# Kernel optimization log

Measured on AMD Instinct MI355X. Metric: run time of the kernel, lower is better.

The kernel has to match this reference:

```python
import jax, jax.numpy as jnp
import numpy as np

N, E = 50000, 400000
FN, FE = 128, 128          # in/out node and edge feature dims
W = 256                     # fnns_width
EPS = 1e-5


def _layer_norm(x, g, b):
    m = x.mean(-1, keepdims=True)
    var = x.var(-1, keepdims=True)
    return (x - m) / jnp.sqrt(var + EPS) * g + b


def _fnn(x, params):
    # FNN applies ReLU after EVERY linear, including the last one.
    for w, b in params:
        x = jax.nn.relu(x @ w + b)
    return x


def setup_inputs() -> dict:
    key = jax.random.key(0)
    ks = jax.random.split(key, 32)
    s = 0.05
    d = {
        'v': jax.random.normal(ks[0], (N, FN), jnp.float32),
        'e': jax.random.normal(ks[1], (E, FE), jnp.float32),
        'edge_index': jax.random.randint(ks[2], (2, E), 0, N, jnp.int32),
        # edge branch: LayerNorm over concat width FE + 2*FN = 384
        'edge_ln_g': jnp.ones((FE + 2 * FN,), jnp.float32),
        'edge_ln_b': jnp.zeros((FE + 2 * FN,), jnp.float32),
        'ew0': jax.random.normal(ks[3], (FE + 2 * FN, W), jnp.float32) * s,
        'eb0': jnp.zeros((W,), jnp.float32),
        'ew1': jax.random.normal(ks[4], (W, W), jnp.float32) * s,
        'eb1': jnp.zeros((W,), jnp.float32),
        'ew2': jax.random.normal(ks[5], (W, FE), jnp.float32) * s,
        'eb2': jnp.zeros((FE,), jnp.float32),
        'edge_linear': jax.random.normal(ks[6], (FE, FE), jnp.float32) * s,
        # node branch: LayerNorm over concat width FE + FN = 256
        'node_ln_g': jnp.ones((FE + FN,), jnp.float32),
        'node_ln_b': jnp.zeros((FE + FN,), jnp.float32),
        'nw0': jax.random.normal(ks[7], (FE + FN, W), jnp.float32) * s,
        'nb0': jnp.zeros((W,), jnp.float32),
        'nw1': jax.random.normal(ks[8], (W, W), jnp.float32) * s,
        'nb1': jnp.zeros((W,), jnp.float32),
        'nw2': jax.random.normal(ks[9], (W, FN), jnp.float32) * s,
        'nb2': jnp.zeros((FN,), jnp.float32),
        'node_linear': jax.random.normal(ks[10], (FN, FN), jnp.float32) * s,
    }
    return d


def reference(v, e, edge_index, edge_ln_g, edge_ln_b, ew0, eb0, ew1, eb1,
              ew2, eb2, edge_linear, node_ln_g, node_ln_b, nw0, nb0, nw1,
              nb1, nw2, nb2, node_linear):
    row, col = edge_index[0], edge_index[1]
    n = v.shape[0]
    # edge update: residual linear + FNN(LayerNorm(concat))
    edge_in = jnp.concatenate([e, v[row], v[col]], axis=-1)  # [E, 384]
    e_new = e @ edge_linear + _fnn(
        _layer_norm(edge_in, edge_ln_g, edge_ln_b),
        [(ew0, eb0), (ew1, eb1), (ew2, eb2)])
    # mean scatter-aggregate over destination nodes (col)
    counts = jax.ops.segment_sum(jnp.ones((e.shape[0],), e.dtype), col,
                                 num_segments=n)
    e_aggr = jax.ops.segment_sum(e_new, col, num_segments=n)
    e_aggr = e_aggr / jnp.clip(counts, 1.0)[:, None]
    # node update
    node_in = jnp.concatenate([e_aggr, v], axis=-1)  # [N, 256]
    v_new = v @ node_linear + _fnn(
        _layer_norm(node_in, node_ln_g, node_ln_b),
        [(nw0, nb0), (nw1, nb1), (nw2, nb2)])
    return (v_new, e_new)
```

## Files before the change

kernel.cpp:

```cpp
#include <hip/hip_runtime.h>

typedef _Float16 f16_t;
typedef f16_t f16x4 __attribute__((ext_vector_type(4)));
typedef f16_t f16x8 __attribute__((ext_vector_type(8)));
typedef float f32x4 __attribute__((ext_vector_type(4)));

#define MFMA16(a, b, c) __builtin_amdgcn_mfma_f32_16x16x32_f16((a), (b), (c), 0, 0, 0)

__device__ __forceinline__ float bfr(float x) { return (float)(__bf16)x; }

__global__ void pack_weights_kernel(
    const float* __restrict__ ew0, const float* __restrict__ ew1,
    const float* __restrict__ ew2, const float* __restrict__ eL,
    const float* __restrict__ nw0, const float* __restrict__ nw1,
    const float* __restrict__ nw2, const float* __restrict__ nL,
    f16_t* __restrict__ dst)
{
    int tid = blockIdx.x * 256 + threadIdx.x;
    int fid = tid >> 6, lane = tid & 63;
    const float* src; int Ncols, foff, doff;
    if (fid < 192)      { src = ew0; Ncols = 256; foff = 0;   doff = 0;      }
    else if (fid < 320) { src = ew1; Ncols = 256; foff = 192; doff = 98304;  }
    else if (fid < 384) { src = ew2; Ncols = 128; foff = 320; doff = 163840; }
    else if (fid < 416) { src = eL;  Ncols = 128; foff = 384; doff = 196608; }
    else if (fid < 544) { src = nw0; Ncols = 256; foff = 416; doff = 212992; }
    else if (fid < 672) { src = nw1; Ncols = 256; foff = 544; doff = 278528; }
    else if (fid < 736) { src = nw2; Ncols = 128; foff = 672; doff = 344064; }
    else                { src = nL;  Ncols = 128; foff = 736; doff = 376832; }
    int f = fid - foff;
    int NT = Ncols >> 4;
    int kstep = f / NT, ntile = f - kstep * NT;
    int col = ntile * 16 + (lane & 15);
    int kbase = kstep * 32 + ((lane >> 4) << 3);
    f16x8 out;
    #pragma unroll
    for (int j = 0; j < 8; ++j)
        out[j] = (f16_t)bfr(src[(size_t)(kbase + j) * Ncols + col]);
    *reinterpret_cast<f16x8*>(dst + (size_t)doff + ((size_t)f * 64 + lane) * 8) = out;
}

__global__ void pack_params_kernel(
    const float* __restrict__ elng, const float* __restrict__ elnb,
    const float* __restrict__ eb0,  const float* __restrict__ eb1,
    const float* __restrict__ eb2,  const float* __restrict__ nlng,
    const float* __restrict__ nlnb, const float* __restrict__ nb0,
    const float* __restrict__ nb1,  const float* __restrict__ nb2,
    float* __restrict__ pp)
{
    int tid = blockIdx.x * 256 + threadIdx.x;
    if (tid >= 2560) return;
    const float* src; int off;
    if (tid < 384)       { src = elng; off = 0; }
    else if (tid < 768)  { src = elnb; off = 384; }
    else if (tid < 1024) { src = eb0;  off = 768; }
    else if (tid < 1280) { src = eb1;  off = 1024; }
    else if (tid < 1408) { src = eb2;  off = 1280; }
    else if (tid < 1664) { src = nlng; off = 1408; }
    else if (tid < 1920) { src = nlnb; off = 1664; }
    else if (tid < 2176) { src = nb0;  off = 1920; }
    else if (tid < 2432) { src = nb1;  off = 2176; }
    else                 { src = nb2;  off = 2432; }
    pp[tid] = bfr(src[tid - off]);
}

__launch_bounds__(1024, 8)
__global__ void edge_kernel(
    const float* __restrict__ vfeat, const float* __restrict__ efeat,
    const int* __restrict__ eidx,
    const float* __restrict__ pp,
    const f16_t* __restrict__ pw,
    float* __restrict__ out_e, float* __restrict__ aggr, float* __restrict__ cnts,
    int Ee)
{
    __shared__ f16_t XF[12 * 4 * 512];
    __shared__ f16_t ERF[4 * 4 * 512];
    __shared__ float SB[64 * 8];
    __shared__ int cidx[64];

    const int t    = threadIdx.x;
    const int lane = t & 63;
    const int wv   = t >> 6;
    const int r16  = lane & 15;
    const int g4i  = lane >> 4;
    const size_t ebase = (size_t)blockIdx.x * 64;

    const int et_  = wv >> 2;
    const int sq4  = wv & 3;
    const int edge = et_ * 16 + r16;
    const int slot = sq4 * 4 + g4i;
    const size_t eg0 = ebase + edge;
    const int r0 = eidx[eg0];
    const int c0 = eidx[(size_t)Ee + eg0];

    f16x8 oct[3];
    float s = 0.f, sq = 0.f;
    {
        const float4* e4 = (const float4*)efeat;
        const float4* v4 = (const float4*)vfeat;
        const float4* srcs[3];
        srcs[0] = &e4[eg0 * 32 + slot * 2];
        srcs[1] = &v4[(size_t)r0 * 32 + slot * 2];
        srcs[2] = &v4[(size_t)c0 * 32 + slot * 2];
        #pragma unroll
        for (int i = 0; i < 3; ++i) {
            float4 f0 = srcs[i][0];
            float4 f1 = srcs[i][1];
            float x0 = bfr(f0.x), x1 = bfr(f0.y), x2 = bfr(f0.z), x3 = bfr(f0.w);
            float x4 = bfr(f1.x), x5 = bfr(f1.y), x6 = bfr(f1.z), x7 = bfr(f1.w);
            s  += x0 + x1 + x2 + x3 + x4 + x5 + x6 + x7;
            sq += x0*x0 + x1*x1 + x2*x2 + x3*x3 + x4*x4 + x5*x5 + x6*x6 + x7*x7;
            f16x8 h;
            h[0] = (f16_t)x0; h[1] = (f16_t)x1; h[2] = (f16_t)x2; h[3] = (f16_t)x3;
            h[4] = (f16_t)x4; h[5] = (f16_t)x5; h[6] = (f16_t)x6; h[7] = (f16_t)x7;
            oct[i] = h;
        }
        *reinterpret_cast<f16x8*>(&ERF[(sq4 * 4 + et_) * 512 + lane * 8]) = oct[0];
        if (slot == 0) {
            cidx[edge] = c0;
            unsafeAtomicAdd(&cnts[c0], 1.0f);
        }
    }
    s  += __shfl_xor(s, 16);  s  += __shfl_xor(s, 32);
    sq += __shfl_xor(sq, 16); sq += __shfl_xor(sq, 32);
    if (g4i == 0)
        *reinterpret_cast<float2*>(&SB[edge * 8 + sq4 * 2]) = make_float2(s, sq);
    __syncthreads();

    {
        float4 p0 = *reinterpret_cast<const float4*>(&SB[edge * 8]);
        float4 p1 = *reinterpret_cast<const float4*>(&SB[edge * 8 + 4]);
        float S = p0.x + p0.z + p1.x + p1.z;
        float Q = p0.y + p0.w + p1.y + p1.w;
        const float mean = S * (1.f / 384.f);
        const float rstd = 1.f / sqrtf(Q * (1.f / 384.f) - mean * mean + 1e-5f);
        const float4* g4p = (const float4*)pp;
        const float4* bpp = (const float4*)(pp + 384);
        #pragma unroll
        for (int i = 0; i < 3; ++i) {
            int q = (i * 16 + slot) * 2;
            float4 g0 = g4p[q], g1 = g4p[q + 1];
            float4 bb0 = bpp[q], bb1 = bpp[q + 1];
            f16x8 h = oct[i];
            f16x8 y;
            float tt, cc;
            tt = rstd * g0.x; cc = bb0.x - mean * tt; y[0] = (f16_t)((float)h[0] * tt + cc);
            tt = rstd * g0.y; cc = bb0.y - mean * tt; y[1] = (f16_t)((float)h[1] * tt + cc);
            tt = rstd * g0.z; cc = bb0.z - mean * tt; y[2] = (f16_t)((float)h[2] * tt + cc);
            tt = rstd * g0.w; cc = bb0.w - mean * tt; y[3] = (f16_t)((float)h[3] * tt + cc);
            tt = rstd * g1.x; cc = bb1.x - mean * tt; y[4] = (f16_t)((float)h[4] * tt + cc);
            tt = rstd * g1.y; cc = bb1.y - mean * tt; y[5] = (f16_t)((float)h[5] * tt + cc);
            tt = rstd * g1.z; cc = bb1.z - mean * tt; y[6] = (f16_t)((float)h[6] * tt + cc);
            tt = rstd * g1.w; cc = bb1.w - mean * tt; y[7] = (f16_t)((float)h[7] * tt + cc);
            int ks = i * 4 + sq4;
            *reinterpret_cast<f16x8*>(&XF[(ks * 4 + et_) * 512 + lane * 8]) = y;
        }
    }
    __syncthreads();

    {
        f32x4 acc[4] = {};
        const f16_t* bw = pw;
        f16x8 wA = *reinterpret_cast<const f16x8*>(&bw[((size_t)(wv) * 64 + lane) * 8]);
        f16x8 wB = *reinterpret_cast<const f16x8*>(&bw[((size_t)(16 + wv) * 64 + lane) * 8]);
        #pragma unroll
        for (int ks = 0; ks < 12; ++ks) {
            f16x8 wN = wB;
            if (ks + 2 < 12)
                wN = *reinterpret_cast<const f16x8*>(
                    &bw[((size_t)((ks + 2) * 16 + wv) * 64 + lane) * 8]);
            #pragma unroll
            for (int et = 0; et < 4; ++et) {
                f16x8 xb = *reinterpret_cast<const f16x8*>(
                    &XF[(ks * 4 + et) * 512 + lane * 8]);
                acc[et] = MFMA16(wA, xb, acc[et]);
            }
            wA = wB; wB = wN;
        }
        __syncthreads();
        float4 bs = *reinterpret_cast<const float4*>(&pp[768 + wv * 16 + g4i * 4]);
        int ks2 = wv >> 1;
        int lane2 = r16 + 16 * ((wv & 1) * 2 + (g4i >> 1));
        int j0 = (g4i & 1) * 4;
        #pragma unroll
        for (int et = 0; et < 4; ++et) {
            f16x4 hv;
            hv[0] = (f16_t)fmaxf(acc[et][0] + bs.x, 0.f);
            hv[1] = (f16_t)fmaxf(acc[et][1] + bs.y, 0.f);
            hv[2] = (f16_t)fmaxf(acc[et][2] + bs.z, 0.f);
            hv[3] = (f16_t)fmaxf(acc[et][3] + bs.w, 0.f);
            *reinterpret_cast<f16x4*>(&XF[(ks2 * 4 + et) * 512 + lane2 * 8 + j0]) = hv;
        }
    }
    __syncthreads();

    {
        f32x4 acc[4] = {};
        const f16_t* bw = pw + 98304;
        f16x8 wA = *reinterpret_cast<const f16x8*>(&bw[((size_t)(wv) * 64 + lane) * 8]);
        f16x8 wB = *reinterpret_cast<const f16x8*>(&bw[((size_t)(16 + wv) * 64 + lane) * 8]);
        #pragma unroll
        for (int ks = 0; ks < 8; ++ks) {
            f16x8 wN = wB;
            if (ks + 2 < 8)
                wN = *reinterpret_cast<const f16x8*>(
                    &bw[((size_t)((ks + 2) * 16 + wv) * 64 + lane) * 8]);
            #pragma unroll
            for (int et = 0; et < 4; ++et) {
                f16x8 xb = *reinterpret_cast<const f16x8*>(
                    &XF[(ks * 4 + et) * 512 + lane * 8]);
                acc[et] = MFMA16(wA, xb, acc[et]);
            }
            wA = wB; wB = wN;
        }
        __syncthreads();
        float4 bs = *reinterpret_cast<const float4*>(&pp[1024 + wv * 16 + g4i * 4]);
        int ks2 = wv >> 1;
        int lane2 = r16 + 16 * ((wv & 1) * 2 + (g4i >> 1));
        int j0 = (g4i & 1) * 4;
        #pragma unroll
        for (int et = 0; et < 4; ++et) {
            f16x4 hv;
            hv[0] = (f16_t)fmaxf(acc[et][0] + bs.x, 0.f);
            hv[1] = (f16_t)fmaxf(acc[et][1] + bs.y, 0.f);
            hv[2] = (f16_t)fmaxf(acc[et][2] + bs.z, 0.f);
            hv[3] = (f16_t)fmaxf(acc[et][3] + bs.w, 0.f);
            *reinterpret_cast<f16x4*>(&XF[(ks2 * 4 + et) * 512 + lane2 * 8 + j0]) = hv;
        }
    }
    __syncthreads();

    {
        const int cw = wv & 7;
        const int rw = wv >> 3;
        f32x4 accF[2] = {}, accR[2] = {};
        const f16_t* bw = pw + 163840;
        f16x8 wA = *reinterpret_cast<const f16x8*>(&bw[((size_t)(cw) * 64 + lane) * 8]);
        f16x8 wB = *reinterpret_cast<const f16x8*>(&bw[((size_t)(8 + cw) * 64 + lane) * 8]);
        #pragma unroll
        for (int ks = 0; ks < 8; ++ks) {
            f16x8 wN = wB;
            if (ks + 2 < 8)
                wN = *reinterpret_cast<const f16x8*>(
                    &bw[((size_t)((ks + 2) * 8 + cw) * 64 + lane) * 8]);
            #pragma unroll
            for (int e2 = 0; e2 < 2; ++e2) {
                f16x8 xa = *reinterpret_cast<const f16x8*>(
                    &XF[(ks * 4 + rw * 2 + e2) * 512 + lane * 8]);
                accF[e2] = MFMA16(xa, wA, accF[e2]);
            }
            wA = wB; wB = wN;
        }
        const f16_t* bwL = pw + 196608;
        f16x8 lA = *reinterpret_cast<const f16x8*>(&bwL[((size_t)(cw) * 64 + lane) * 8]);
        f16x8 lB = *reinterpret_cast<const f16x8*>(&bwL[((size_t)(8 + cw) * 64 + lane) * 8]);
        #pragma unroll
        for (int ks = 0; ks < 4; ++ks) {
            f16x8 lN = lB;
            if (ks + 2 < 4)
                lN = *reinterpret_cast<const f16x8*>(
                    &bwL[((size_t)((ks + 2) * 8 + cw) * 64 + lane) * 8]);
            #pragma unroll
            for (int e2 = 0; e2 < 2; ++e2) {
                f16x8 ea = *reinterpret_cast<const f16x8*>(
                    &ERF[(ks * 4 + rw * 2 + e2) * 512 + lane * 8]);
                accR[e2] = MFMA16(ea, lA, accR[e2]);
            }
            lA = lB; lB = lN;
        }
        int c = cw * 16 + r16;
        float bias = pp[1280 + c];
        #pragma unroll
        for (int e2 = 0; e2 < 2; ++e2)
            #pragma unroll
            for (int qi = 0; qi < 4; ++qi) {
                int rr = (rw * 2 + e2) * 16 + g4i * 4 + qi;
                float val = accR[e2][qi] + fmaxf(accF[e2][qi] + bias, 0.f);
                size_t eg2 = ebase + rr;
                out_e[eg2 * 128 + c] = val;
                unsafeAtomicAdd(&aggr[(size_t)cidx[rr] * 128 + c], val);
            }
    }
}

__launch_bounds__(512, 6)
__global__ void node_kernel(
    const float* __restrict__ vfeat, const float* __restrict__ aggr,
    const float* __restrict__ cnts,
    const float* __restrict__ pp,
    const f16_t* __restrict__ pw,
    float* __restrict__ out_v, int Nn)
{
    __shared__ f16_t X[32 * 264];
    __shared__ f16_t H1[32 * 264];

    const int t    = threadIdx.x;
    const int lane = t & 63;
    const int wv   = t >> 6;
    const size_t nbase = (size_t)blockIdx.x * 32;

    const int nl = t >> 4;
    const int pp16 = t & 15;
    const size_t ng = nbase + nl;
    const bool valid = ng < (size_t)Nn;

    float4 d[4];
    float s = 0.f, sq = 0.f;
    {
        float cmax = 1.f;
        if (valid) cmax = fmaxf(cnts[ng], 1.f);
        const float4* a4 = (const float4*)aggr;
        const float4* v4 = (const float4*)vfeat;
        #pragma unroll
        for (int i = 0; i < 4; ++i) {
            int q = i * 16 + pp16;
            float4 r = make_float4(0.f, 0.f, 0.f, 0.f);
            if (valid) {
                if (q < 32) {
                    r = a4[ng * 32 + q];
                    r.x = r.x / cmax; r.y = r.y / cmax;
                    r.z = r.z / cmax; r.w = r.w / cmax;
                } else {
                    float4 rv = v4[ng * 32 + (q - 32)];
                    r.x = bfr(rv.x); r.y = bfr(rv.y); r.z = bfr(rv.z); r.w = bfr(rv.w);
                }
            }
            d[i] = r;
            s  += r.x + r.y + r.z + r.w;
            sq += r.x*r.x + r.y*r.y + r.z*r.z + r.w*r.w;
        }
    }
    #pragma unroll
    for (int off = 1; off < 16; off <<= 1) {
        s  += __shfl_xor(s, off);
        sq += __shfl_xor(sq, off);
    }
    const float mean = s * (1.f / 256.f);
    const float rstd = 1.f / sqrtf(sq * (1.f / 256.f) - mean * mean + 1e-5f);
    {
        const float4* g4p = (const float4*)(pp + 1408);
        const float4* bpp = (const float4*)(pp + 1664);
        #pragma unroll
        for (int i = 0; i < 4; ++i) {
            int q = i * 16 + pp16;
            float4 g = g4p[q]; float4 bb = bpp[q];
            f16x4 y;
            float tt;
            tt = rstd * g.x; y[0] = (f16_t)(d[i].x * tt + (bb.x - mean * tt));
            tt = rstd * g.y; y[1] = (f16_t)(d[i].y * tt + (bb.y - mean * tt));
            tt = rstd * g.z; y[2] = (f16_t)(d[i].z * tt + (bb.z - mean * tt));
            tt = rstd * g.w; y[3] = (f16_t)(d[i].w * tt + (bb.w - mean * tt));
            *reinterpret_cast<f16x4*>(&X[nl * 264 + q * 4]) = y;
        }
    }
    __syncthreads();

    const int r16 = lane & 15;
    const int g4i = lane >> 4;
    const int cb4 = g4i * 4;

    {
        f32x4 acc[2][2] = {};
        const f16_t* bw = pw;
        #pragma unroll
        for (int ks = 0; ks < 8; ++ks) {
            f16x8 wa0 = *reinterpret_cast<const f16x8*>(
                &bw[((size_t)(ks * 16 + wv * 2 + 0) * 64 + lane) * 8]);
            f16x8 wa1 = *reinterpret_cast<const f16x8*>(
                &bw[((size_t)(ks * 16 + wv * 2 + 1) * 64 + lane) * 8]);
            #pragma unroll
            for (int nt = 0; nt < 2; ++nt) {
                f16x8 xb = *reinterpret_cast<const f16x8*>(
                    &X[(nt * 16 + r16) * 264 + ks * 32 + g4i * 8]);
                acc[nt][0] = MFMA16(wa0, xb, acc[nt][0]);
                acc[nt][1] = MFMA16(wa1, xb, acc[nt][1]);
            }
        }
        #pragma unroll
        for (int j = 0; j < 2; ++j) {
            int cb = (wv * 2 + j) * 16 + cb4;
            float4 bs = *reinterpret_cast<const float4*>(&pp[1920 + cb]);
            #pragma unroll
            for (int nt = 0; nt < 2; ++nt) {
                f16x4 hv;
                hv[0] = (f16_t)fmaxf(acc[nt][j][0] + bs.x, 0.f);
                hv[1] = (f16_t)fmaxf(acc[nt][j][1] + bs.y, 0.f);
                hv[2] = (f16_t)fmaxf(acc[nt][j][2] + bs.z, 0.f);
                hv[3] = (f16_t)fmaxf(acc[nt][j][3] + bs.w, 0.f);
                *reinterpret_cast<f16x4*>(&H1[(nt * 16 + r16) * 264 + cb]) = hv;
            }
        }
    }
    __syncthreads();

    {
        f32x4 acc[2][2] = {};
        const f16_t* bw = pw + 65536;
        #pragma unroll
        for (int ks = 0; ks < 8; ++ks) {
            f16x8 wa0 = *reinterpret_cast<const f16x8*>(
                &bw[((size_t)(ks * 16 + wv * 2 + 0) * 64 + lane) * 8]);
            f16x8 wa1 = *reinterpret_cast<const f16x8*>(
                &bw[((size_t)(ks * 16 + wv * 2 + 1) * 64 + lane) * 8]);
            #pragma unroll
            for (int nt = 0; nt < 2; ++nt) {
                f16x8 xb = *reinterpret_cast<const f16x8*>(
                    &H1[(nt * 16 + r16) * 264 + ks * 32 + g4i * 8]);
                acc[nt][0] = MFMA16(wa0, xb, acc[nt][0]);
                acc[nt][1] = MFMA16(wa1, xb, acc[nt][1]);
            }
        }
        __syncthreads();
        #pragma unroll
        for (int j = 0; j < 2; ++j) {
            int cb = (wv * 2 + j) * 16 + cb4;
            float4 bs = *reinterpret_cast<const float4*>(&pp[2176 + cb]);
            #pragma unroll
            for (int nt = 0; nt < 2; ++nt) {
                f16x4 hv;
                hv[0] = (f16_t)fmaxf(acc[nt][j][0] + bs.x, 0.f);
                hv[1] = (f16_t)fmaxf(acc[nt][j][1] + bs.y, 0.f);
                hv[2] = (f16_t)fmaxf(acc[nt][j][2] + bs.z, 0.f);
                hv[3] = (f16_t)fmaxf(acc[nt][j][3] + bs.w, 0.f);
                *reinterpret_cast<f16x4*>(&X[(nt * 16 + r16) * 264 + cb]) = hv;
            }
        }
    }
    __syncthreads();

    {
        f32x4 accF[2] = {}, accR[2] = {};
        const f16_t* bw = pw + 131072;
        #pragma unroll
        for (int ks = 0; ks < 8; ++ks) {
            f16x8 wb = *reinterpret_cast<const f16x8*>(
                &bw[((size_t)(ks * 8 + wv) * 64 + lane) * 8]);
            #pragma unroll
            for (int nt = 0; nt < 2; ++nt) {
                f16x8 xa = *reinterpret_cast<const f16x8*>(
                    &X[(nt * 16 + r16) * 264 + ks * 32 + g4i * 8]);
                accF[nt] = MFMA16(xa, wb, accF[nt]);
            }
        }
        const f16_t* bwL = pw + 163840;
        #pragma unroll
        for (int ks = 0; ks < 4; ++ks) {
            f16x8 wb = *reinterpret_cast<const f16x8*>(
                &bwL[((size_t)(ks * 8 + wv) * 64 + lane) * 8]);
            #pragma unroll
            for (int nt = 0; nt < 2; ++nt) {
                size_t rv = nbase + (size_t)(nt * 16 + r16);
                if (rv >= (size_t)Nn) rv = (size_t)Nn - 1;
                const float4* src = (const float4*)&vfeat[rv * 128 + ks * 32 + g4i * 8];
                float4 f0 = src[0];
                float4 f1 = src[1];
                f16x8 va;
                va[0] = (f16_t)bfr(f0.x); va[1] = (f16_t)bfr(f0.y);
                va[2] = (f16_t)bfr(f0.z); va[3] = (f16_t)bfr(f0.w);
                va[4] = (f16_t)bfr(f1.x); va[5] = (f16_t)bfr(f1.y);
                va[6] = (f16_t)bfr(f1.z); va[7] = (f16_t)bfr(f1.w);
                accR[nt] = MFMA16(va, wb, accR[nt]);
            }
        }
        int c = wv * 16 + r16;
        float bias = pp[2432 + c];
        #pragma unroll
        for (int nt = 0; nt < 2; ++nt)
            #pragma unroll
            for (int qi = 0; qi < 4; ++qi) {
                int rr = nt * 16 + cb4 + qi;
                size_t ng2 = nbase + rr;
                if (ng2 < (size_t)Nn) {
                    float val = accR[nt][qi] + fmaxf(accF[nt][qi] + bias, 0.f);
                    out_v[ng2 * 128 + c] = val;
                }
            }
    }
}

extern "C" void kernel_launch(void* const* d_in, const int* in_sizes, int n_in,
                              void* d_out, int out_size, void* d_ws, size_t ws_size,
                              hipStream_t stream)
{
    const float* v    = (const float*)d_in[0];
    const float* e    = (const float*)d_in[1];
    const int*   eidx = (const int*)d_in[2];
    const float* elng = (const float*)d_in[3];
    const float* elnb = (const float*)d_in[4];
    const float* ew0  = (const float*)d_in[5];
    const float* eb0  = (const float*)d_in[6];
    const float* ew1  = (const float*)d_in[7];
    const float* eb1  = (const float*)d_in[8];
    const float* ew2  = (const float*)d_in[9];
    const float* eb2  = (const float*)d_in[10];
    const float* eLin = (const float*)d_in[11];
    const float* nlng = (const float*)d_in[12];
    const float* nlnb = (const float*)d_in[13];
    const float* nw0  = (const float*)d_in[14];
    const float* nb0  = (const float*)d_in[15];
    const float* nw1  = (const float*)d_in[16];
    const float* nb1  = (const float*)d_in[17];
    const float* nw2  = (const float*)d_in[18];
    const float* nb2  = (const float*)d_in[19];
    const float* nLin = (const float*)d_in[20];

    const int Nn = in_sizes[0] / 128;
    const int Ee = in_sizes[1] / 128;

    float* out_v = (float*)d_out;
    float* out_e = out_v + (size_t)Nn * 128;

    float* aggr = (float*)d_ws;
    float* cnts = aggr + (size_t)Nn * 128;
    f16_t* packw = (f16_t*)((char*)d_ws + (size_t)Nn * 129 * 4);
    float* pp = (float*)((char*)packw + 393216 * 2);

    hipMemsetAsync(d_ws, 0, (size_t)Nn * 129 * 4, stream);

    pack_weights_kernel<<<192, 256, 0, stream>>>(ew0, ew1, ew2, eLin,
                                                 nw0, nw1, nw2, nLin, packw);
    pack_params_kernel<<<10, 256, 0, stream>>>(elng, elnb, eb0, eb1, eb2,
                                               nlng, nlnb, nb0, nb1, nb2, pp);

    edge_kernel<<<(Ee + 63) / 64, 1024, 0, stream>>>(v, e, eidx, pp, packw,
                                                     out_e, aggr, cnts, Ee);

    node_kernel<<<(Nn + 31) / 32, 512, 0, stream>>>(v, aggr, cnts, pp,
                                                    packw + 212992, out_v, Nn);
}
```

Measured before the change: 434.7 us.

## Switch 256-wide MLP layers to 32x32x16 MFMA with fragment-packed LDS layout

Repacks the weights of the two 256-output layers (edge and node) into a 32x32x16 MFMA fragment format and rewrites those GEMMs to use a single 32x32 accumulator per wave instead of several 16x16 tiles. The edge LayerNorm now uses 16 consecutive threads per edge, so the reduction stays within shuffles and the shared-memory partial-sum buffer plus its barrier go away. The node kernel's LDS staging is changed from padded row-major to the MFMA fragment layout, and the explicit weight register double-buffering is removed. The aim is fewer MFMA issues, fewer LDS reads and one fewer barrier, at the cost of different register pressure and the loss of manual weight prefetching.

```diff
diff --git a/kernel.cpp b/kernel.cpp
--- a/kernel.cpp
+++ b/kernel.cpp
@@ -4,10 +4,14 @@
 typedef f16_t f16x4 __attribute__((ext_vector_type(4)));
 typedef f16_t f16x8 __attribute__((ext_vector_type(8)));
 typedef float f32x4 __attribute__((ext_vector_type(4)));
-
-#define MFMA16(a, b, c) __builtin_amdgcn_mfma_f32_16x16x32_f16((a), (b), (c), 0, 0, 0)
+typedef float f32x16 __attribute__((ext_vector_type(16)));
+
+#define MFMA16(a,b,c) __builtin_amdgcn_mfma_f32_16x16x32_f16((a),(b),(c),0,0,0)
+#define MFMA32(a,b,c) __builtin_amdgcn_mfma_f32_32x32x16_f16((a),(b),(c),0,0,0)
 
 __device__ __forceinline__ float bfr(float x) { return (float)(__bf16)x; }
+
+#define ACC16_ZERO {0.f,0.f,0.f,0.f,0.f,0.f,0.f,0.f,0.f,0.f,0.f,0.f,0.f,0.f,0.f,0.f}
 
 __global__ void pack_weights_kernel(
     const float* __restrict__ ew0, const float* __restrict__ ew1,
@@ -18,20 +22,28 @@
 {
     int tid = blockIdx.x * 256 + threadIdx.x;
     int fid = tid >> 6, lane = tid & 63;
-    const float* src; int Ncols, foff, doff;
-    if (fid < 192)      { src = ew0; Ncols = 256; foff = 0;   doff = 0;      }
-    else if (fid < 320) { src = ew1; Ncols = 256; foff = 192; doff = 98304;  }
-    else if (fid < 384) { src = ew2; Ncols = 128; foff = 320; doff = 163840; }
-    else if (fid < 416) { src = eL;  Ncols = 128; foff = 384; doff = 196608; }
-    else if (fid < 544) { src = nw0; Ncols = 256; foff = 416; doff = 212992; }
-    else if (fid < 672) { src = nw1; Ncols = 256; foff = 544; doff = 278528; }
-    else if (fid < 736) { src = nw2; Ncols = 128; foff = 672; doff = 344064; }
-    else                { src = nL;  Ncols = 128; foff = 736; doff = 376832; }
+    const float* src; int Ncols, foff, doff, fmt32;
+    if (fid < 192)      { src = ew0; Ncols = 256; foff = 0;   doff = 0;      fmt32 = 1; }
+    else if (fid < 320) { src = ew1; Ncols = 256; foff = 192; doff = 98304;  fmt32 = 1; }
+    else if (fid < 384) { src = ew2; Ncols = 128; foff = 320; doff = 163840; fmt32 = 0; }
+    else if (fid < 416) { src = eL;  Ncols = 128; foff = 384; doff = 196608; fmt32 = 0; }
+    else if (fid < 544) { src = nw0; Ncols = 256; foff = 416; doff = 212992; fmt32 = 1; }
+    else if (fid < 672) { src = nw1; Ncols = 256; foff = 544; doff = 278528; fmt32 = 1; }
+    else if (fid < 736) { src = nw2; Ncols = 128; foff = 672; doff = 344064; fmt32 = 0; }
+    else                { src = nL;  Ncols = 128; foff = 736; doff = 376832; fmt32 = 0; }
     int f = fid - foff;
-    int NT = Ncols >> 4;
-    int kstep = f / NT, ntile = f - kstep * NT;
-    int col = ntile * 16 + (lane & 15);
-    int kbase = kstep * 32 + ((lane >> 4) << 3);
+    int col, kbase;
+    if (fmt32) {
+        int NT = Ncols >> 5;
+        int ks = f / NT, nt = f - ks * NT;
+        col = nt * 32 + (lane & 31);
+        kbase = ks * 16 + ((lane >> 5) << 3);
+    } else {
+        int NT = Ncols >> 4;
+        int ks = f / NT, nt = f - ks * NT;
+        col = nt * 16 + (lane & 15);
+        kbase = ks * 32 + ((lane >> 4) << 3);
+    }
     f16x8 out;
     #pragma unroll
     for (int j = 0; j < 8; ++j)
@@ -72,22 +84,17 @@
     float* __restrict__ out_e, float* __restrict__ aggr, float* __restrict__ cnts,
     int Ee)
 {
-    __shared__ f16_t XF[12 * 4 * 512];
-    __shared__ f16_t ERF[4 * 4 * 512];
-    __shared__ float SB[64 * 8];
+    __shared__ f16_t XF[48 * 512];
+    __shared__ f16_t ERF[16 * 512];
     __shared__ int cidx[64];
 
     const int t    = threadIdx.x;
     const int lane = t & 63;
     const int wv   = t >> 6;
-    const int r16  = lane & 15;
-    const int g4i  = lane >> 4;
     const size_t ebase = (size_t)blockIdx.x * 64;
 
-    const int et_  = wv >> 2;
-    const int sq4  = wv & 3;
-    const int edge = et_ * 16 + r16;
-    const int slot = sq4 * 4 + g4i;
+    const int edge = t >> 4;
+    const int slot = t & 15;
     const size_t eg0 = ebase + edge;
     const int r0 = eidx[eg0];
     const int c0 = eidx[(size_t)Ee + eg0];
@@ -114,27 +121,26 @@
             h[4] = (f16_t)x4; h[5] = (f16_t)x5; h[6] = (f16_t)x6; h[7] = (f16_t)x7;
             oct[i] = h;
         }
-        *reinterpret_cast<f16x8*>(&ERF[(sq4 * 4 + et_) * 512 + lane * 8]) = oct[0];
+        int fe = (slot >> 2) * 4 + (edge >> 4);
+        int lane16 = (edge & 15) + 16 * (slot & 3);
+        *reinterpret_cast<f16x8*>(&ERF[fe * 512 + lane16 * 8]) = oct[0];
         if (slot == 0) {
             cidx[edge] = c0;
             unsafeAtomicAdd(&cnts[c0], 1.0f);
         }
     }
-    s  += __shfl_xor(s, 16);  s  += __shfl_xor(s, 32);
-    sq += __shfl_xor(sq, 16); sq += __shfl_xor(sq, 32);
-    if (g4i == 0)
-        *reinterpret_cast<float2*>(&SB[edge * 8 + sq4 * 2]) = make_float2(s, sq);
-    __syncthreads();
-
-    {
-        float4 p0 = *reinterpret_cast<const float4*>(&SB[edge * 8]);
-        float4 p1 = *reinterpret_cast<const float4*>(&SB[edge * 8 + 4]);
-        float S = p0.x + p0.z + p1.x + p1.z;
-        float Q = p0.y + p0.w + p1.y + p1.w;
-        const float mean = S * (1.f / 384.f);
-        const float rstd = 1.f / sqrtf(Q * (1.f / 384.f) - mean * mean + 1e-5f);
+    s  += __shfl_xor(s, 1);  s  += __shfl_xor(s, 2);
+    s  += __shfl_xor(s, 4);  s  += __shfl_xor(s, 8);
+    sq += __shfl_xor(sq, 1); sq += __shfl_xor(sq, 2);
+    sq += __shfl_xor(sq, 4); sq += __shfl_xor(sq, 8);
+    const float mean = s * (1.f / 384.f);
+    const float rstd = 1.f / sqrtf(sq * (1.f / 384.f) - mean * mean + 1e-5f);
+
+    {
         const float4* g4p = (const float4*)pp;
         const float4* bpp = (const float4*)(pp + 384);
+        const int et = edge >> 5;
+        const int lane32 = (edge & 31) + 32 * (slot & 1);
         #pragma unroll
         for (int i = 0; i < 3; ++i) {
             int q = (i * 16 + slot) * 2;
@@ -151,80 +157,70 @@
             tt = rstd * g1.y; cc = bb1.y - mean * tt; y[5] = (f16_t)((float)h[5] * tt + cc);
             tt = rstd * g1.z; cc = bb1.z - mean * tt; y[6] = (f16_t)((float)h[6] * tt + cc);
             tt = rstd * g1.w; cc = bb1.w - mean * tt; y[7] = (f16_t)((float)h[7] * tt + cc);
-            int ks = i * 4 + sq4;
-            *reinterpret_cast<f16x8*>(&XF[(ks * 4 + et_) * 512 + lane * 8]) = y;
+            int ks = i * 8 + (slot >> 1);
+            *reinterpret_cast<f16x8*>(&XF[(ks * 2 + et) * 512 + lane32 * 8]) = y;
         }
     }
     __syncthreads();
 
-    {
-        f32x4 acc[4] = {};
+    const int el31 = lane & 31;
+    const int h2b  = lane >> 5;
+
+    {
+        const int c8 = wv & 7, rh = wv >> 3;
+        f32x16 acc = ACC16_ZERO;
         const f16_t* bw = pw;
-        f16x8 wA = *reinterpret_cast<const f16x8*>(&bw[((size_t)(wv) * 64 + lane) * 8]);
-        f16x8 wB = *reinterpret_cast<const f16x8*>(&bw[((size_t)(16 + wv) * 64 + lane) * 8]);
-        #pragma unroll
-        for (int ks = 0; ks < 12; ++ks) {
-            f16x8 wN = wB;
-            if (ks + 2 < 12)
-                wN = *reinterpret_cast<const f16x8*>(
-                    &bw[((size_t)((ks + 2) * 16 + wv) * 64 + lane) * 8]);
-            #pragma unroll
-            for (int et = 0; et < 4; ++et) {
-                f16x8 xb = *reinterpret_cast<const f16x8*>(
-                    &XF[(ks * 4 + et) * 512 + lane * 8]);
-                acc[et] = MFMA16(wA, xb, acc[et]);
-            }
-            wA = wB; wB = wN;
+        #pragma unroll
+        for (int ks = 0; ks < 24; ++ks) {
+            f16x8 wa = *reinterpret_cast<const f16x8*>(
+                &bw[((size_t)(ks * 8 + c8) * 64 + lane) * 8]);
+            f16x8 xb = *reinterpret_cast<const f16x8*>(
+                &XF[(ks * 2 + rh) * 512 + lane * 8]);
+            acc = MFMA32(wa, xb, acc);
         }
         __syncthreads();
-        float4 bs = *reinterpret_cast<const float4*>(&pp[768 + wv * 16 + g4i * 4]);
-        int ks2 = wv >> 1;
-        int lane2 = r16 + 16 * ((wv & 1) * 2 + (g4i >> 1));
-        int j0 = (g4i & 1) * 4;
-        #pragma unroll
-        for (int et = 0; et < 4; ++et) {
+        #pragma unroll
+        for (int c = 0; c < 4; ++c) {
+            int oc0 = c8 * 32 + 8 * c + 4 * h2b;
+            float4 bs = *reinterpret_cast<const float4*>(&pp[768 + oc0]);
             f16x4 hv;
-            hv[0] = (f16_t)fmaxf(acc[et][0] + bs.x, 0.f);
-            hv[1] = (f16_t)fmaxf(acc[et][1] + bs.y, 0.f);
-            hv[2] = (f16_t)fmaxf(acc[et][2] + bs.z, 0.f);
-            hv[3] = (f16_t)fmaxf(acc[et][3] + bs.w, 0.f);
-            *reinterpret_cast<f16x4*>(&XF[(ks2 * 4 + et) * 512 + lane2 * 8 + j0]) = hv;
+            hv[0] = (f16_t)fmaxf(acc[4*c+0] + bs.x, 0.f);
+            hv[1] = (f16_t)fmaxf(acc[4*c+1] + bs.y, 0.f);
+            hv[2] = (f16_t)fmaxf(acc[4*c+2] + bs.z, 0.f);
+            hv[3] = (f16_t)fmaxf(acc[4*c+3] + bs.w, 0.f);
+            int frag = (c8 * 2 + (c >> 1)) * 2 + rh;
+            *reinterpret_cast<f16x4*>(
+                &XF[frag * 512 + (el31 + 32 * (c & 1)) * 8 + 4 * h2b]) = hv;
         }
     }
     __syncthreads();
 
     {
-        f32x4 acc[4] = {};
+        const int c8 = wv & 7, rh = wv >> 3;
+        f32x16 acc = ACC16_ZERO;
         const f16_t* bw = pw + 98304;
-        f16x8 wA = *reinterpret_cast<const f16x8*>(&bw[((size_t)(wv) * 64 + lane) * 8]);
-        f16x8 wB = *reinterpret_cast<const f16x8*>(&bw[((size_t)(16 + wv) * 64 + lane) * 8]);
-        #pragma unroll
-        for (int ks = 0; ks < 8; ++ks) {
-            f16x8 wN = wB;
-            if (ks + 2 < 8)
-                wN = *reinterpret_cast<const f16x8*>(
-                    &bw[((size_t)((ks + 2) * 16 + wv) * 64 + lane) * 8]);
-            #pragma unroll
-            for (int et = 0; et < 4; ++et) {
-                f16x8 xb = *reinterpret_cast<const f16x8*>(
-                    &XF[(ks * 4 + et) * 512 + lane * 8]);
-                acc[et] = MFMA16(wA, xb, acc[et]);
-            }
-            wA = wB; wB = wN;
+        #pragma unroll
+        for (int ks = 0; ks < 16; ++ks) {
+            f16x8 wa = *reinterpret_cast<const f16x8*>(
+                &bw[((size_t)(ks * 8 + c8) * 64 + lane) * 8]);
+            f16x8 xb = *reinterpret_cast<const f16x8*>(
+                &XF[(ks * 2 + rh) * 512 + lane * 8]);
+            acc = MFMA32(wa, xb, acc);
         }
         __syncthreads();
-        float4 bs = *reinterpret_cast<const float4*>(&pp[1024 + wv * 16 + g4i * 4]);
-        int ks2 = wv >> 1;
-        int lane2 = r16 + 16 * ((wv & 1) * 2 + (g4i >> 1));
-        int j0 = (g4i & 1) * 4;
-        #pragma unroll
-        for (int et = 0; et < 4; ++et) {
+        const int eg16 = rh * 32 + el31;
+        #pragma unroll
+        for (int c = 0; c < 4; ++c) {
+            int oc0 = c8 * 32 + 8 * c + 4 * h2b;
+            float4 bs = *reinterpret_cast<const float4*>(&pp[1024 + oc0]);
             f16x4 hv;
-            hv[0] = (f16_t)fmaxf(acc[et][0] + bs.x, 0.f);
-            hv[1] = (f16_t)fmaxf(acc[et][1] + bs.y, 0.f);
-            hv[2] = (f16_t)fmaxf(acc[et][2] + bs.z, 0.f);
-            hv[3] = (f16_t)fmaxf(acc[et][3] + bs.w, 0.f);
-            *reinterpret_cast<f16x4*>(&XF[(ks2 * 4 + et) * 512 + lane2 * 8 + j0]) = hv;
+            hv[0] = (f16_t)fmaxf(acc[4*c+0] + bs.x, 0.f);
+            hv[1] = (f16_t)fmaxf(acc[4*c+1] + bs.y, 0.f);
+            hv[2] = (f16_t)fmaxf(acc[4*c+2] + bs.z, 0.f);
+            hv[3] = (f16_t)fmaxf(acc[4*c+3] + bs.w, 0.f);
+            int frag = c8 * 4 + (eg16 >> 4);
+            *reinterpret_cast<f16x4*>(
+                &XF[frag * 512 + ((eg16 & 15) + 16 * c) * 8 + 4 * h2b]) = hv;
         }
     }
     __syncthreads();
@@ -232,40 +228,32 @@
     {
         const int cw = wv & 7;
         const int rw = wv >> 3;
+        const int r16 = lane & 15;
+        const int g4i = lane >> 4;
         f32x4 accF[2] = {}, accR[2] = {};
         const f16_t* bw = pw + 163840;
-        f16x8 wA = *reinterpret_cast<const f16x8*>(&bw[((size_t)(cw) * 64 + lane) * 8]);
-        f16x8 wB = *reinterpret_cast<const f16x8*>(&bw[((size_t)(8 + cw) * 64 + lane) * 8]);
         #pragma unroll
         for (int ks = 0; ks < 8; ++ks) {
-            f16x8 wN = wB;
-            if (ks + 2 < 8)
-                wN = *reinterpret_cast<const f16x8*>(
-                    &bw[((size_t)((ks + 2) * 8 + cw) * 64 + lane) * 8]);
+            f16x8 wb = *reinterpret_cast<const f16x8*>(
+                &bw[((size_t)(ks * 8 + cw) * 64 + lane) * 8]);
             #pragma unroll
             for (int e2 = 0; e2 < 2; ++e2) {
                 f16x8 xa = *reinterpret_cast<const f16x8*>(
                     &XF[(ks * 4 + rw * 2 + e2) * 512 + lane * 8]);
-                accF[e2] = MFMA16(xa, wA, accF[e2]);
-            }
-            wA = wB; wB = wN;
+                accF[e2] = MFMA16(xa, wb, accF[e2]);
+            }
         }
         const f16_t* bwL = pw + 196608;
-        f16x8 lA = *reinterpret_cast<const f16x8*>(&bwL[((size_t)(cw) * 64 + lane) * 8]);
-        f16x8 lB = *reinterpret_cast<const f16x8*>(&bwL[((size_t)(8 + cw) * 64 + lane) * 8]);
         #pragma unroll
         for (int ks = 0; ks < 4; ++ks) {
-            f16x8 lN = lB;
-            if (ks + 2 < 4)
-                lN = *reinterpret_cast<const f16x8*>(
-                    &bwL[((size_t)((ks + 2) * 8 + cw) * 64 + lane) * 8]);
+            f16x8 wb = *reinterpret_cast<const f16x8*>(
+                &bwL[((size_t)(ks * 8 + cw) * 64 + lane) * 8]);
             #pragma unroll
             for (int e2 = 0; e2 < 2; ++e2) {
                 f16x8 ea = *reinterpret_cast<const f16x8*>(
                     &ERF[(ks * 4 + rw * 2 + e2) * 512 + lane * 8]);
-                accR[e2] = MFMA16(ea, lA, accR[e2]);
-            }
-            lA = lB; lB = lN;
+                accR[e2] = MFMA16(ea, wb, accR[e2]);
+            }
         }
         int c = cw * 16 + r16;
         float bias = pp[1280 + c];
@@ -290,144 +278,140 @@
     const f16_t* __restrict__ pw,
     float* __restrict__ out_v, int Nn)
 {
-    __shared__ f16_t X[32 * 264];
-    __shared__ f16_t H1[32 * 264];
+    __shared__ f16_t XF[16 * 512];
+    __shared__ f16_t H1[16 * 512];
 
     const int t    = threadIdx.x;
     const int lane = t & 63;
     const int wv   = t >> 6;
     const size_t nbase = (size_t)blockIdx.x * 32;
 
-    const int nl = t >> 4;
-    const int pp16 = t & 15;
+    const int nl   = t >> 4;
+    const int slot = t & 15;
     const size_t ng = nbase + nl;
     const bool valid = ng < (size_t)Nn;
 
-    float4 d[4];
+    f16x8 oct[2];
     float s = 0.f, sq = 0.f;
     {
-        float cmax = 1.f;
-        if (valid) cmax = fmaxf(cnts[ng], 1.f);
+        float inv = 1.f;
+        if (valid) inv = 1.f / fmaxf(cnts[ng], 1.f);
         const float4* a4 = (const float4*)aggr;
         const float4* v4 = (const float4*)vfeat;
         #pragma unroll
-        for (int i = 0; i < 4; ++i) {
-            int q = i * 16 + pp16;
-            float4 r = make_float4(0.f, 0.f, 0.f, 0.f);
+        for (int i = 0; i < 2; ++i) {
+            float x0=0.f,x1=0.f,x2=0.f,x3=0.f,x4=0.f,x5=0.f,x6=0.f,x7=0.f;
             if (valid) {
-                if (q < 32) {
-                    r = a4[ng * 32 + q];
-                    r.x = r.x / cmax; r.y = r.y / cmax;
-                    r.z = r.z / cmax; r.w = r.w / cmax;
+                const float4* srcp = (i == 0) ? &a4[ng * 32 + slot * 2]
+                                              : &v4[ng * 32 + slot * 2];
+                float4 f0 = srcp[0], f1 = srcp[1];
+                if (i == 0) {
+                    x0 = f0.x*inv; x1 = f0.y*inv; x2 = f0.z*inv; x3 = f0.w*inv;
+                    x4 = f1.x*inv; x5 = f1.y*inv; x6 = f1.z*inv; x7 = f1.w*inv;
                 } else {
-                    float4 rv = v4[ng * 32 + (q - 32)];
-                    r.x = bfr(rv.x); r.y = bfr(rv.y); r.z = bfr(rv.z); r.w = bfr(rv.w);
+                    x0 = bfr(f0.x); x1 = bfr(f0.y); x2 = bfr(f0.z); x3 = bfr(f0.w);
+                    x4 = bfr(f1.x); x5 = bfr(f1.y); x6 = bfr(f1.z); x7 = bfr(f1.w);
                 }
             }
-            d[i] = r;
-            s  += r.x + r.y + r.z + r.w;
-            sq += r.x*r.x + r.y*r.y + r.z*r.z + r.w*r.w;
-        }
-    }
-    #pragma unroll
-    for (int off = 1; off < 16; off <<= 1) {
-        s  += __shfl_xor(s, off);
-        sq += __shfl_xor(sq, off);
-    }
+            s  += x0 + x1 + x2 + x3 + x4 + x5 + x6 + x7;
+            sq += x0*x0 + x1*x1 + x2*x2 + x3*x3 + x4*x4 + x5*x5 + x6*x6 + x7*x7;
+            f16x8 h;
+            h[0] = (f16_t)x0; h[1] = (f16_t)x1; h[2] = (f16_t)x2; h[3] = (f16_t)x3;
+            h[4] = (f16_t)x4; h[5] = (f16_t)x5; h[6] = (f16_t)x6; h[7] = (f16_t)x7;
+            oct[i] = h;
+        }
+    }
+    s  += __shfl_xor(s, 1);  s  += __shfl_xor(s, 2);
+    s  += __shfl_xor(s, 4);  s  += __shfl_xor(s, 8);
+    sq += __shfl_xor(sq, 1); sq += __shfl_xor(sq, 2);
+    sq += __shfl_xor(sq, 4); sq += __shfl_xor(sq, 8);
     const float mean = s * (1.f / 256.f);
     const float rstd = 1.f / sqrtf(sq * (1.f / 256.f) - mean * mean + 1e-5f);
+
     {
         const float4* g4p = (const float4*)(pp + 1408);
         const float4* bpp = (const float4*)(pp + 1664);
-        #pragma unroll
-        for (int i = 0; i < 4; ++i) {
-            int q = i * 16 + pp16;
-            float4 g = g4p[q]; float4 bb = bpp[q];
-            f16x4 y;
-            float tt;
-            tt = rstd * g.x; y[0] = (f16_t)(d[i].x * tt + (bb.x - mean * tt));
-            tt = rstd * g.y; y[1] = (f16_t)(d[i].y * tt + (bb.y - mean * tt));
-            tt = rstd * g.z; y[2] = (f16_t)(d[i].z * tt + (bb.z - mean * tt));
-            tt = rstd * g.w; y[3] = (f16_t)(d[i].w * tt + (bb.w - mean * tt));
-            *reinterpret_cast<f16x4*>(&X[nl * 264 + q * 4]) = y;
+        const int lane32 = nl + 32 * (slot & 1);
+        #pragma unroll
+        for (int i = 0; i < 2; ++i) {
+            int q = (i * 16 + slot) * 2;
+            float4 g0 = g4p[q], g1 = g4p[q + 1];
+            float4 bb0 = bpp[q], bb1 = bpp[q + 1];
+            f16x8 h = oct[i];
+            f16x8 y;
+            float tt, cc;
+            tt = rstd * g0.x; cc = bb0.x - mean * tt; y[0] = (f16_t)((float)h[0] * tt + cc);
+            tt = rstd * g0.y; cc = bb0.y - mean * tt; y[1] = (f16_t)((float)h[1] * tt + cc);
+            tt = rstd * g0.z; cc = bb0.z - mean * tt; y[2] = (f16_t)((float)h[2] * tt + cc);
+            tt = rstd * g0.w; cc = bb0.w - mean * tt; y[3] = (f16_t)((float)h[3] * tt + cc);
+            tt = rstd * g1.x; cc = bb1.x - mean * tt; y[4] = (f16_t)((float)h[4] * tt + cc);
+            tt = rstd * g1.y; cc = bb1.y - mean * tt; y[5] = (f16_t)((float)h[5] * tt + cc);
+            tt = rstd * g1.z; cc = bb1.z - mean * tt; y[6] = (f16_t)((float)h[6] * tt + cc);
+            tt = rstd * g1.w; cc = bb1.w - mean * tt; y[7] = (f16_t)((float)h[7] * tt + cc);
+            int ks = i * 8 + (slot >> 1);
+            *reinterpret_cast<f16x8*>(&XF[ks * 512 + lane32 * 8]) = y;
         }
     }
     __syncthreads();
 
-    const int r16 = lane & 15;
-    const int g4i = lane >> 4;
-    const int cb4 = g4i * 4;
-
-    {
-        f32x4 acc[2][2] = {};
+    const int n31 = lane & 31;
+    const int h2b = lane >> 5;
+
+    {
+        f32x16 acc = ACC16_ZERO;
         const f16_t* bw = pw;
         #pragma unroll
-        for (int ks = 0; ks < 8; ++ks) {
-            f16x8 wa0 = *reinterpret_cast<const f16x8*>(
-                &bw[((size_t)(ks * 16 + wv * 2 + 0) * 64 + lane) * 8]);
-            f16x8 wa1 = *reinterpret_cast<const f16x8*>(
-                &bw[((size_t)(ks * 16 + wv * 2 + 1) * 64 + lane) * 8]);
-            #pragma unroll
-            for (int nt = 0; nt < 2; ++nt) {
-                f16x8 xb = *reinterpret_cast<const f16x8*>(
-                    &X[(nt * 16 + r16) * 264 + ks * 32 + g4i * 8]);
-                acc[nt][0] = MFMA16(wa0, xb, acc[nt][0]);
-                acc[nt][1] = MFMA16(wa1, xb, acc[nt][1]);
-            }
-        }
-        #pragma unroll
-        for (int j = 0; j < 2; ++j) {
-            int cb = (wv * 2 + j) * 16 + cb4;
-            float4 bs = *reinterpret_cast<const float4*>(&pp[1920 + cb]);
-            #pragma unroll
-            for (int nt = 0; nt < 2; ++nt) {
-                f16x4 hv;
-                hv[0] = (f16_t)fmaxf(acc[nt][j][0] + bs.x, 0.f);
-                hv[1] = (f16_t)fmaxf(acc[nt][j][1] + bs.y, 0.f);
-                hv[2] = (f16_t)fmaxf(acc[nt][j][2] + bs.z, 0.f);
-                hv[3] = (f16_t)fmaxf(acc[nt][j][3] + bs.w, 0.f);
-                *reinterpret_cast<f16x4*>(&H1[(nt * 16 + r16) * 264 + cb]) = hv;
-            }
+        for (int ks = 0; ks < 16; ++ks) {
+            f16x8 wa = *reinterpret_cast<const f16x8*>(
+                &bw[((size_t)(ks * 8 + wv) * 64 + lane) * 8]);
+            f16x8 xb = *reinterpret_cast<const f16x8*>(&XF[ks * 512 + lane * 8]);
+            acc = MFMA32(wa, xb, acc);
+        }
+        #pragma unroll
+        for (int c = 0; c < 4; ++c) {
+            int oc0 = wv * 32 + 8 * c + 4 * h2b;
+            float4 bs = *reinterpret_cast<const float4*>(&pp[1920 + oc0]);
+            f16x4 hv;
+            hv[0] = (f16_t)fmaxf(acc[4*c+0] + bs.x, 0.f);
+            hv[1] = (f16_t)fmaxf(acc[4*c+1] + bs.y, 0.f);
+            hv[2] = (f16_t)fmaxf(acc[4*c+2] + bs.z, 0.f);
+            hv[3] = (f16_t)fmaxf(acc[4*c+3] + bs.w, 0.f);
+            int frag = wv * 2 + (c >> 1);
+            *reinterpret_cast<f16x4*>(
+                &H1[frag * 512 + (n31 + 32 * (c & 1)) * 8 + 4 * h2b]) = hv;
         }
     }
     __syncthreads();
 
     {
-        f32x4 acc[2][2] = {};
+        f32x16 acc = ACC16_ZERO;
         const f16_t* bw = pw + 65536;
         #pragma unroll
-        for (int ks = 0; ks < 8; ++ks) {
-            f16x8 wa0 = *reinterpret_cast<const f16x8*>(
-                &bw[((size_t)(ks * 16 + wv * 2 + 0) * 64 + lane) * 8]);
-            f16x8 wa1 = *reinterpret_cast<const f16x8*>(
-                &bw[((size_t)(ks * 16 + wv * 2 + 1) * 64 + lane) * 8]);
-            #pragma unroll
-            for (int nt = 0; nt < 2; ++nt) {
-                f16x8 xb = *reinterpret_cast<const f16x8*>(
-                    &H1[(nt * 16 + r16) * 264 + ks * 32 + g4i * 8]);
-                acc[nt][0] = MFMA16(wa0, xb, acc[nt][0]);
-                acc[nt][1] = MFMA16(wa1, xb, acc[nt][1]);
-            }
-        }
-        __syncthreads();
-        #pragma unroll
-        for (int j = 0; j < 2; ++j) {
-            int cb = (wv * 2 + j) * 16 + cb4;
-            float4 bs = *reinterpret_cast<const float4*>(&pp[2176 + cb]);
-            #pragma unroll
-            for (int nt = 0; nt < 2; ++nt) {
-                f16x4 hv;
-                hv[0] = (f16_t)fmaxf(acc[nt][j][0] + bs.x, 0.f);
-                hv[1] = (f16_t)fmaxf(acc[nt][j][1] + bs.y, 0.f);
-                hv[2] = (f16_t)fmaxf(acc[nt][j][2] + bs.z, 0.f);
-                hv[3] = (f16_t)fmaxf(acc[nt][j][3] + bs.w, 0.f);
-                *reinterpret_cast<f16x4*>(&X[(nt * 16 + r16) * 264 + cb]) = hv;
-            }
+        for (int ks = 0; ks < 16; ++ks) {
+            f16x8 wa = *reinterpret_cast<const f16x8*>(
+                &bw[((size_t)(ks * 8 + wv) * 64 + lane) * 8]);
+            f16x8 xb = *reinterpret_cast<const f16x8*>(&H1[ks * 512 + lane * 8]);
+            acc = MFMA32(wa, xb, acc);
+        }
+        #pragma unroll
+        for (int c = 0; c < 4; ++c) {
+            int oc0 = wv * 32 + 8 * c + 4 * h2b;
+            float4 bs = *reinterpret_cast<const float4*>(&pp[2176 + oc0]);
+            f16x4 hv;
+            hv[0] = (f16_t)fmaxf(acc[4*c+0] + bs.x, 0.f);
+            hv[1] = (f16_t)fmaxf(acc[4*c+1] + bs.y, 0.f);
+            hv[2] = (f16_t)fmaxf(acc[4*c+2] + bs.z, 0.f);
+            hv[3] = (f16_t)fmaxf(acc[4*c+3] + bs.w, 0.f);
+            int frag = wv * 2 + (n31 >> 4);
+            *reinterpret_cast<f16x4*>(
+                &XF[frag * 512 + ((n31 & 15) + 16 * c) * 8 + 4 * h2b]) = hv;
         }
     }
     __syncthreads();
 
     {
+        const int r16 = lane & 15;
+        const int g4i = lane >> 4;
         f32x4 accF[2] = {}, accR[2] = {};
         const f16_t* bw = pw + 131072;
         #pragma unroll
@@ -437,7 +421,7 @@
             #pragma unroll
             for (int nt = 0; nt < 2; ++nt) {
                 f16x8 xa = *reinterpret_cast<const f16x8*>(
-                    &X[(nt * 16 + r16) * 264 + ks * 32 + g4i * 8]);
+                    &XF[(ks * 2 + nt) * 512 + lane * 8]);
                 accF[nt] = MFMA16(xa, wb, accF[nt]);
             }
         }
@@ -467,7 +451,7 @@
         for (int nt = 0; nt < 2; ++nt)
             #pragma unroll
             for (int qi = 0; qi < 4; ++qi) {
-                int rr = nt * 16 + cb4 + qi;
+                int rr = nt * 16 + g4i * 4 + qi;
                 size_t ng2 = nbase + rr;
                 if (ng2 < (size_t)Nn) {
                     float val = accR[nt][qi] + fmaxf(accF[nt][qi] + bias, 0.f);
```

Measured after the change: 535.6 us. 23.2% more time.
